# Performance work log

Hardware: AMD Instinct MI355X
Metric: run time of the kernel (lower is better)

## Reference

```python
import jax, jax.numpy as jnp
import numpy as np

EPS_LN = 1e-5  # torch nn.LayerNorm default

def layernorm(x, g, b):
    mu = x.mean(-1, keepdims=True)
    var = ((x - mu) ** 2).mean(-1, keepdims=True)
    return (x - mu) * jax.lax.rsqrt(var + EPS_LN) * g + b

def softmax_kernel(x, proj, is_query, kernel_eps=1e-4):
    # FAVOR+ positive softmax random features (performer_pytorch math).
    # x: (B,H,N,D) queries/keys, proj: (M,D) random projection.
    d = x.shape[-1]
    norm = d ** -0.25
    ratio = proj.shape[0] ** -0.5
    xd = jnp.einsum('bhnd,md->bhnm', x * norm, proj)
    diag = 0.5 * (x ** 2).sum(-1, keepdims=True) * (norm ** 2)  # (B,H,N,1)
    stab = jnp.max(xd, axis=-1, keepdims=True) if is_query else jnp.max(xd)
    return ratio * (jnp.exp(xd - diag - stab) + kernel_eps)

def linear_attention(q, k, v):
    # Non-causal O(N) attention. q,k: (B,H,N,M); v: (B,H,N,DH)
    k_sum = k.sum(axis=-2)                                      # (B,H,M)
    d_inv = 1.0 / jnp.einsum('bhnm,bhm->bhn', q, k_sum)
    context = jnp.einsum('bhnm,bhnd->bhmd', k, v)               # (B,H,M,DH)
    return jnp.einsum('bhnm,bhmd,bhn->bhnd', q, context, d_inv)

def setup_inputs():
    key = jax.random.key(0)
    B, K, D, H, L = 32, 2048, 256, 4, 2
    DH = D // H
    M = int(DH * np.log(DH))  # 266, performer_pytorch default nb_features
    FF = 4 * D
    ks = jax.random.split(key, 20)
    def w(i, shape):
        return jax.random.normal(ks[i], shape, dtype=jnp.float32) * 0.02
    return dict(
        expr=jax.random.uniform(ks[0], (B, K), dtype=jnp.float32),
        coords=jax.random.uniform(ks[1], (B, 2), dtype=jnp.float32),
        gene_emb=w(2, (K, D)), pos_emb=w(3, (K, D)),
        val_w=w(4, (1, D)), val_b=jnp.zeros((D,), jnp.float32),
        val_ln_g=jnp.ones((D,), jnp.float32), val_ln_b=jnp.zeros((D,), jnp.float32),
        sp_w=w(5, (2, D)), sp_b=jnp.zeros((D,), jnp.float32),
        sp_ln_g=jnp.ones((D,), jnp.float32), sp_ln_b=jnp.zeros((D,), jnp.float32),
        p_ln1_g=jnp.ones((L, D), jnp.float32), p_ln1_b=jnp.zeros((L, D), jnp.float32),
        p_wq=w(6, (L, D, D)), p_bq=jnp.zeros((L, D), jnp.float32),
        p_wk=w(7, (L, D, D)), p_bk=jnp.zeros((L, D), jnp.float32),
        p_wv=w(8, (L, D, D)), p_bv=jnp.zeros((L, D), jnp.float32),
        p_wo=w(9, (L, D, D)), p_bo=jnp.zeros((L, D), jnp.float32),
        p_ln2_g=jnp.ones((L, D), jnp.float32), p_ln2_b=jnp.zeros((L, D), jnp.float32),
        p_ff1_w=w(10, (L, D, FF)), p_ff1_b=jnp.zeros((L, FF), jnp.float32),
        p_ff2_w=w(11, (L, FF, D)), p_ff2_b=jnp.zeros((L, D), jnp.float32),
        proj=jax.random.normal(ks[12], (L, M, DH), dtype=jnp.float32),
        q_w=w(13, (D, D)), q_b=jnp.zeros((D,), jnp.float32),
        k_w=w(14, (D, D)), k_b=jnp.zeros((D,), jnp.float32),
        v_w=w(15, (D, D)), v_b=jnp.zeros((D,), jnp.float32),
        o_w=w(16, (D, D)), o_b=jnp.zeros((D,), jnp.float32),
    )

def reference(expr, coords, gene_emb, pos_emb, val_w, val_b, val_ln_g, val_ln_b,
              sp_w, sp_b, sp_ln_g, sp_ln_b,
              p_ln1_g, p_ln1_b, p_wq, p_bq, p_wk, p_bk, p_wv, p_bv, p_wo, p_bo,
              p_ln2_g, p_ln2_b, p_ff1_w, p_ff1_b, p_ff2_w, p_ff2_b, proj,
              q_w, q_b, k_w, k_b, v_w, v_b, o_w, o_b):
    B, K = expr.shape
    D = gene_emb.shape[1]
    L = p_wq.shape[0]
    H = 4
    DH = D // H
    # gene tokens = gene_id_emb + gene_pos_emb + GELU(LN(Linear(expr)))
    val = jax.nn.gelu(layernorm(expr[..., None] * val_w[0] + val_b, val_ln_g, val_ln_b), approximate=False)
    gene_tokens = (gene_emb + pos_emb)[None] + val                      # (B,K,D)
    sp = jax.nn.gelu(layernorm(coords @ sp_w + sp_b, sp_ln_g, sp_ln_b), approximate=False)
    x = jnp.concatenate([sp[:, None, :], gene_tokens], axis=1)          # (B,K+1,D)
    N = K + 1
    def split_heads(t):
        return t.reshape(B, N, H, DH).transpose(0, 2, 1, 3)
    # Performer: depth x [x + Attn(LN(x)); x + FF(LN(x))], dropout off (eval)
    for l in range(L):
        y = layernorm(x, p_ln1_g[l], p_ln1_b[l])
        q = split_heads(y @ p_wq[l] + p_bq[l])
        k = split_heads(y @ p_wk[l] + p_bk[l])
        v = split_heads(y @ p_wv[l] + p_bv[l])
        qf = softmax_kernel(q, proj[l], True)
        kf = softmax_kernel(k, proj[l], False)
        o = linear_attention(qf, kf, v)                                 # (B,H,N,DH)
        o = o.transpose(0, 2, 1, 3).reshape(B, N, D)
        x = x + (o @ p_wo[l] + p_bo[l])
        y = layernorm(x, p_ln2_g[l], p_ln2_b[l])
        x = x + (jax.nn.gelu(y @ p_ff1_w[l] + p_ff1_b[l], approximate=False) @ p_ff2_w[l] + p_ff2_b[l])
    # single-query cross-attention pooling: spatial token attends to genes
    spatial_out = x[:, :1]
    gene_out = x[:, 1:]
    q = spatial_out @ q_w + q_b                                          # (B,1,D)
    kk = gene_out @ k_w + k_b                                            # (B,K,D)
    vv = gene_out @ v_w + v_b
    attn = jax.nn.softmax(jnp.einsum('bqd,bkd->bqk', q, kk) / (D ** 0.5), axis=-1)
    pooled = jnp.einsum('bqk,bkd->bqd', attn, vv)[:, 0]                  # (B,D)
    return pooled @ o_w + o_b
```

## Files before the change

### kernel.cpp

```cpp
#include <hip/hip_runtime.h>
#include <hip/hip_bf16.h>
#include <math.h>

#define NB   32
#define KG   2048
#define NSEQ 2049
#define DIM  256
#define NH   4
#define DH   64
#define MF   266
#define FFD  1024
#define BN   (NB*NSEQ)
#define FFROWS2 32784
#define NORMC 0.35355339059327376f
#define RATIOC (1.0f/16.309506430300091f)

typedef __attribute__((ext_vector_type(8))) short short8;
typedef __attribute__((ext_vector_type(4))) float f32x4;
#define MFMA16(a,b,c) __builtin_amdgcn_mfma_f32_16x16x32_bf16(a,b,c,0,0,0)

__device__ __forceinline__ short f2b(float f){
  union{ __hip_bfloat16 h; short s;} u; u.h = __float2bfloat16(f); return u.s;
}
__device__ __forceinline__ float b2f(short s){
  union{ short s; __hip_bfloat16 h;} u; u.s = s; return __bfloat162float(u.h);
}
__device__ __forceinline__ float gelu_f(float x){
  return 0.5f*x*(1.0f+erff(x*0.70710678118654752f));
}
__device__ __forceinline__ void gload16(const short* g, short* l){
  __builtin_amdgcn_global_load_lds(
      (const __attribute__((address_space(1))) void*)g,
      (__attribute__((address_space(3))) void*)l, 16, 0, 0);
}
__device__ __forceinline__ float waveSum(float v){
  #pragma unroll
  for(int o=32;o>0;o>>=1) v += __shfl_down(v,o);
  return v;
}
__device__ __forceinline__ float waveMax(float v){
  #pragma unroll
  for(int o=32;o>0;o>>=1) v = fmaxf(v,__shfl_down(v,o));
  return v;
}
__device__ __forceinline__ float xorSum64(float v){
  v += __shfl_xor(v,32); v += __shfl_xor(v,16); v += __shfl_xor(v,8);
  v += __shfl_xor(v,4);  v += __shfl_xor(v,2);  v += __shfl_xor(v,1);
  return v;
}
__device__ __forceinline__ float blockSum256(float v, float* red){
  int lane = threadIdx.x & 63, wid = threadIdx.x >> 6;
  v = waveSum(v);
  __syncthreads();
  if(lane==0) red[wid]=v;
  __syncthreads();
  return red[0]+red[1]+red[2]+red[3];
}
__device__ __forceinline__ float blockMax256(float v, float* red){
  int lane = threadIdx.x & 63, wid = threadIdx.x >> 6;
  v = waveMax(v);
  __syncthreads();
  if(lane==0) red[wid]=v;
  __syncthreads();
  return fmaxf(fmaxf(red[0],red[1]),fmaxf(red[2],red[3]));
}
__device__ __forceinline__ unsigned fenc(float f){
  unsigned u = __float_as_uint(f);
  return (u & 0x80000000u) ? ~u : (u | 0x80000000u);
}
__device__ __forceinline__ float fdec(unsigned u){
  return (u & 0x80000000u) ? __uint_as_float(u & 0x7FFFFFFFu) : __uint_as_float(~u);
}

__global__ __launch_bounds__(256) void embed_kernel(
    const float* __restrict__ expr, const float* __restrict__ coords,
    const float* __restrict__ gene_emb, const float* __restrict__ pos_emb,
    const float* __restrict__ val_w, const float* __restrict__ val_b,
    const float* __restrict__ val_g, const float* __restrict__ val_bb,
    const float* __restrict__ sp_w, const float* __restrict__ sp_b,
    const float* __restrict__ sp_g, const float* __restrict__ sp_bb,
    const float* __restrict__ ln_g, const float* __restrict__ ln_b,
    float* __restrict__ x, short* __restrict__ ybf){
  int w = threadIdx.x >> 6, l = threadIdx.x & 63;
  int row = blockIdx.x*4 + w;
  int b = row / NSEQ, n = row % NSEQ;
  int d0 = l*4;
  float4 v;
  if(n==0){
    float c0 = coords[b*2], c1 = coords[b*2+1];
    float4 w0 = *reinterpret_cast<const float4*>(sp_w + d0);
    float4 w1 = *reinterpret_cast<const float4*>(sp_w + DIM + d0);
    float4 bb = *reinterpret_cast<const float4*>(sp_b + d0);
    v = make_float4(c0*w0.x+c1*w1.x+bb.x, c0*w0.y+c1*w1.y+bb.y,
                    c0*w0.z+c1*w1.z+bb.z, c0*w0.w+c1*w1.w+bb.w);
  } else {
    float e = expr[(size_t)b*KG + (n-1)];
    float4 vw = *reinterpret_cast<const float4*>(val_w + d0);
    float4 vb = *reinterpret_cast<const float4*>(val_b + d0);
    v = make_float4(e*vw.x+vb.x, e*vw.y+vb.y, e*vw.z+vb.z, e*vw.w+vb.w);
  }
  float mu = xorSum64(v.x+v.y+v.z+v.w)*(1.0f/DIM);
  float cx=v.x-mu, cy=v.y-mu, cz=v.z-mu, cw=v.w-mu;
  float var = xorSum64(cx*cx+cy*cy+cz*cz+cw*cw)*(1.0f/DIM);
  float r = rsqrtf(var + 1e-5f);
  float4 g  = (n==0)? *reinterpret_cast<const float4*>(sp_g + d0)
                    : *reinterpret_cast<const float4*>(val_g + d0);
  float4 be = (n==0)? *reinterpret_cast<const float4*>(sp_bb + d0)
                    : *reinterpret_cast<const float4*>(val_bb + d0);
  float4 h = make_float4(gelu_f(cx*r*g.x+be.x), gelu_f(cy*r*g.y+be.y),
                         gelu_f(cz*r*g.z+be.z), gelu_f(cw*r*g.w+be.w));
  if(n!=0){
    float4 ge = *reinterpret_cast<const float4*>(gene_emb + (size_t)(n-1)*DIM + d0);
    float4 pe = *reinterpret_cast<const float4*>(pos_emb  + (size_t)(n-1)*DIM + d0);
    h.x += ge.x+pe.x; h.y += ge.y+pe.y; h.z += ge.z+pe.z; h.w += ge.w+pe.w;
  }
  *reinterpret_cast<float4*>(x + (size_t)row*DIM + d0) = h;
  float s2 = xorSum64(h.x+h.y+h.z+h.w);
  float mu2 = s2*(1.0f/DIM);
  float c2x=h.x-mu2, c2y=h.y-mu2, c2z=h.z-mu2, c2w=h.w-mu2;
  float var2 = xorSum64(c2x*c2x+c2y*c2y+c2z*c2z+c2w*c2w)*(1.0f/DIM);
  float r2 = rsqrtf(var2+1e-5f);
  const float4 gv = *reinterpret_cast<const float4*>(ln_g + d0);
  const float4 bv = *reinterpret_cast<const float4*>(ln_b + d0);
  short4 o = make_short4(f2b(c2x*r2*gv.x+bv.x), f2b(c2y*r2*gv.y+bv.y),
                         f2b(c2z*r2*gv.z+bv.z), f2b(c2w*r2*gv.w+bv.w));
  *reinterpret_cast<short4*>(ybf + (size_t)row*DIM + d0) = o;
}

__global__ __launch_bounds__(256) void ln_bf4(const float* __restrict__ xin,
    const float* __restrict__ g, const float* __restrict__ bb, short* __restrict__ ybf){
  int w = threadIdx.x >> 6, l = threadIdx.x & 63;
  int row = blockIdx.x*4 + w;
  const float* xr = xin + (size_t)row*DIM;
  float4 v = *reinterpret_cast<const float4*>(xr + l*4);
  float s = xorSum64(v.x+v.y+v.z+v.w);
  float mu = s*(1.0f/DIM);
  float cx=v.x-mu, cy=v.y-mu, cz=v.z-mu, cw=v.w-mu;
  float var = xorSum64(cx*cx+cy*cy+cz*cz+cw*cw)*(1.0f/DIM);
  float r = rsqrtf(var+1e-5f);
  const float4 gv = *reinterpret_cast<const float4*>(g + l*4);
  const float4 bv = *reinterpret_cast<const float4*>(bb + l*4);
  short4 o = make_short4(f2b(cx*r*gv.x+bv.x), f2b(cy*r*gv.y+bv.y),
                         f2b(cz*r*gv.z+bv.z), f2b(cw*r*gv.w+bv.w));
  *reinterpret_cast<short4*>(ybf + (size_t)row*DIM + l*4) = o;
}

#define NW 14
struct WPArgs {
  const float* src[NW];
  short* dst[NW];
  int K[NW], N[NW];
  int ts[NW+1];
};
__global__ __launch_bounds__(256) void wprep_fused(WPArgs a){
  __shared__ float tile[32][33];
  int bx = blockIdx.x, t = threadIdx.x;
  int i = 0;
  while(bx >= a.ts[i+1]) i++;
  int tl = bx - a.ts[i];
  int N = a.N[i], K = a.K[i];
  int tcols = N >> 5;
  int tr = tl / tcols, tc = tl - tr*tcols;
  const float* src = a.src[i];
  short* dst = a.dst[i];
  int r = t>>3, c4 = (t&7)*4;
  float4 v = *reinterpret_cast<const float4*>(src + (size_t)(tr*32+r)*N + tc*32 + c4);
  tile[r][c4+0]=v.x; tile[r][c4+1]=v.y; tile[r][c4+2]=v.z; tile[r][c4+3]=v.w;
  __syncthreads();
  short4 o = make_short4(f2b(tile[c4+0][r]), f2b(tile[c4+1][r]),
                         f2b(tile[c4+2][r]), f2b(tile[c4+3][r]));
  *reinterpret_cast<short4*>(dst + (size_t)(tc*32+r)*K + tr*32 + c4) = o;
}

template<int EPI, int OBF, int WBF>
__global__ __launch_bounds__(256) void mgemm2(
    const short* __restrict__ A, const short* __restrict__ Bt,
    const float* __restrict__ bias, void* __restrict__ Cv,
    int M, int N, int Kd, short* __restrict__ Yb){
  __shared__ short As[128*64];
  __shared__ short Bs[128*64];
  int t=threadIdx.x, l=t&63, w=t>>6, lr=l&15, lk=l>>4;
  int wm=w>>1, wn=w&1;
  int m0=blockIdx.y*128, n0=blockIdx.x*128;
  f32x4 acc[4][4];
  #pragma unroll
  for(int i=0;i<4;i++)
    #pragma unroll
    for(int j=0;j<4;j++) acc[i][j]=f32x4{0.f,0.f,0.f,0.f};
  int rsw = (l>>3)&7;
  for(int k0=0;k0<Kd;k0+=64){
    #pragma unroll
    for(int p=0;p<4;p++){
      int chunk = p*256 + t;
      int row = chunk>>3, qc = chunk&7;
      short* lbase = &As[(size_t)(p*256 + w*64)*8];
      gload16(A + (size_t)(m0+row)*Kd + k0 + (qc^rsw)*8, lbase);
    }
    #pragma unroll
    for(int p=0;p<4;p++){
      int chunk = p*256 + t;
      int row = chunk>>3, qc = chunk&7;
      short* lbase = &Bs[(size_t)(p*256 + w*64)*8];
      gload16(Bt + (size_t)(n0+row)*Kd + k0 + (qc^rsw)*8, lbase);
    }
    __syncthreads();
    #pragma unroll
    for(int ks=0;ks<2;ks++){
      short8 af[4], bfr[4];
      #pragma unroll
      for(int i=0;i<4;i++)
        af[i] = *reinterpret_cast<const short8*>(&As[(wm*64+i*16+lr)*64 + ((ks*32+lk*8)^((lr&7)<<3))]);
      #pragma unroll
      for(int j=0;j<4;j++)
        bfr[j] = *reinterpret_cast<const short8*>(&Bs[(wn*64+j*16+lr)*64 + ((ks*32+lk*8)^((lr&7)<<3))]);
      #pragma unroll
      for(int i=0;i<4;i++)
        #pragma unroll
        for(int j=0;j<4;j++) acc[i][j] = MFMA16(af[i], bfr[j], acc[i][j]);
    }
    __syncthreads();
  }
  #pragma unroll
  for(int i=0;i<4;i++){
    int gm0 = m0 + wm*64 + i*16 + lk*4;
    #pragma unroll
    for(int j=0;j<4;j++){
      int gc = n0 + wn*64 + j*16 + lr;
      float bs = bias[gc];
      #pragma unroll
      for(int r=0;r<4;r++){
        int gm = gm0 + r;
        if(gm<M){
          float vv = acc[i][j][r] + bs;
          if(EPI==2) vv = gelu_f(vv);
          size_t idx = (size_t)gm*N + gc;
          if(OBF){
            ((short*)Cv)[idx] = f2b(vv);
          } else {
            float* C = (float*)Cv;
            if(EPI==1) vv += C[idx];
            C[idx] = vv;
            if(WBF) Yb[idx] = f2b(vv);
          }
        }
      }
    }
  }
}

__global__ __launch_bounds__(256) void qkv_gemm(
    const short* __restrict__ A, const short* __restrict__ Bt,
    const float* __restrict__ bq, const float* __restrict__ bk, const float* __restrict__ bv,
    short* __restrict__ qd, short* __restrict__ kd, short* __restrict__ vd,
    float* __restrict__ diagk, int M){
  __shared__ short As[128*64];
  __shared__ short Bs[128*64];
  int t=threadIdx.x, l=t&63, w=t>>6, lr=l&15, lk=l>>4;
  int wm=w>>1, wn=w&1;
  int m0=blockIdx.y*128, n0=blockIdx.x*128;
  f32x4 acc[4][4];
  #pragma unroll
  for(int i=0;i<4;i++)
    #pragma unroll
    for(int j=0;j<4;j++) acc[i][j]=f32x4{0.f,0.f,0.f,0.f};
  int rsw = (l>>3)&7;
  for(int k0=0;k0<DIM;k0+=64){
    #pragma unroll
    for(int p=0;p<4;p++){
      int chunk = p*256 + t;
      int row = chunk>>3, qc = chunk&7;
      short* lbase = &As[(size_t)(p*256 + w*64)*8];
      gload16(A + (size_t)(m0+row)*DIM + k0 + (qc^rsw)*8, lbase);
    }
    #pragma unroll
    for(int p=0;p<4;p++){
      int chunk = p*256 + t;
      int row = chunk>>3, qc = chunk&7;
      short* lbase = &Bs[(size_t)(p*256 + w*64)*8];
      gload16(Bt + (size_t)(n0+row)*DIM + k0 + (qc^rsw)*8, lbase);
    }
    __syncthreads();
    #pragma unroll
    for(int ks=0;ks<2;ks++){
      short8 af[4], bfr[4];
      #pragma unroll
      for(int i=0;i<4;i++)
        af[i] = *reinterpret_cast<const short8*>(&As[(wm*64+i*16+lr)*64 + ((ks*32+lk*8)^((lr&7)<<3))]);
      #pragma unroll
      for(int j=0;j<4;j++)
        bfr[j] = *reinterpret_cast<const short8*>(&Bs[(wn*64+j*16+lr)*64 + ((ks*32+lk*8)^((lr&7)<<3))]);
      #pragma unroll
      for(int i=0;i<4;i++)
        #pragma unroll
        for(int j=0;j<4;j++) acc[i][j] = MFMA16(af[i], bfr[j], acc[i][j]);
    }
    __syncthreads();
  }
  bool isK = (blockIdx.x==2) || (blockIdx.x==3);
  int headq = ((n0 + wn*64) - 256) >> 6;
  #pragma unroll
  for(int i=0;i<4;i++){
    int gm0 = m0 + wm*64 + i*16 + lk*4;
    float sq[4] = {0.f,0.f,0.f,0.f};
    #pragma unroll
    for(int j=0;j<4;j++){
      int gc = n0 + wn*64 + j*16 + lr;
      int sel = gc >> 8, col = gc & 255;
      short* dst = (sel==0)? qd : ((sel==1)? kd : vd);
      const float* bp = (sel==0)? bq : ((sel==1)? bk : bv);
      float bs = bp[col];
      #pragma unroll
      for(int r=0;r<4;r++){
        int gm = gm0 + r;
        if(gm<M){
          short sv = f2b(acc[i][j][r] + bs);
          dst[(size_t)gm*DIM + col] = sv;
          if(isK){ float kv = b2f(sv); sq[r] += kv*kv; }
        }
      }
    }
    if(isK){
      #pragma unroll
      for(int r=0;r<4;r++){
        float s = sq[r];
        s += __shfl_xor(s,1); s += __shfl_xor(s,2);
        s += __shfl_xor(s,4); s += __shfl_xor(s,8);
        if(lr==0){
          int gm = gm0 + r;
          if(gm<M){
            int bb_ = gm / NSEQ, nn_ = gm - bb_*NSEQ;
            diagk[((size_t)(bb_*NH+headq))*NSEQ + nn_] = 0.0625f*s;
          }
        }
      }
    }
  }
}

__global__ __launch_bounds__(256) void projprep_kernel(const float* __restrict__ proj,
    short* __restrict__ projbf, unsigned* __restrict__ kmax){
  int i = blockIdx.x*256 + threadIdx.x;
  if(i==0) *kmax = 0u;
  if(i < 320*64){
    int m = i>>6, d = i&63;
    float v = (m<MF)? proj[(size_t)m*DH + d]*NORMC : 0.f;
    projbf[i] = f2b(v);
  }
}

__global__ __launch_bounds__(256) void kside_max(
    const short* __restrict__ kbf, const short* __restrict__ projbf,
    unsigned* __restrict__ kmax){
  __shared__ short kS[32*72];
  __shared__ float red[4];
  int t=threadIdx.x, l=t&63, w=t>>6, lr=l&15, lk=l>>4;
  int split = blockIdx.x, bh = blockIdx.y;
  int b=bh>>2, h=bh&3;
  int c0 = split*9, c1 = min(c0+9, 65);
  int nf = (w==3)?5:4;
  short8 apf[5][2];
  #pragma unroll
  for(int fi=0;fi<5;fi++){
    int fr = (fi<4)? (fi*4+w) : 16;
    #pragma unroll
    for(int ks=0;ks<2;ks++)
      apf[fi][ks] = *reinterpret_cast<const short8*>(projbf + (fr*16+lr)*64 + ks*32 + lk*8);
  }
  const short8 z8 = {0,0,0,0,0,0,0,0};
  float lmax = -3.0e38f;
  for(int ch=c0; ch<c1; ++ch){
    int n0 = ch*32;
    __syncthreads();
    {
      int r = t>>3, c8 = (t&7)*8;
      int gn = n0 + r;
      short8 v8 = z8;
      if(gn<NSEQ) v8 = *reinterpret_cast<const short8*>(kbf + ((size_t)(b*NSEQ+gn))*DIM + h*DH + c8);
      *reinterpret_cast<short8*>(&kS[r*72+c8]) = v8;
    }
    __syncthreads();
    for(int fi=0;fi<nf;fi++){
      int fr = (fi<4)? (fi*4+w) : 16;
      #pragma unroll
      for(int fn=0;fn<2;fn++){
        f32x4 xa = f32x4{0.f,0.f,0.f,0.f};
        #pragma unroll
        for(int ks=0;ks<2;ks++){
          short8 bk = *reinterpret_cast<const short8*>(&kS[(fn*16+lr)*72 + ks*32 + lk*8]);
          xa = MFMA16(apf[fi][ks], bk, xa);
        }
        #pragma unroll
        for(int r=0;r<4;r++){
          int m = fr*16 + lk*4 + r;
          int n = n0 + fn*16 + lr;
          if(m<MF && n<NSEQ) lmax = fmaxf(lmax, xa[r]);
        }
      }
    }
  }
  float bm = blockMax256(lmax, red);
  if(t==0) atomicMax(kmax, fenc(bm));
}

__global__ __launch_bounds__(256) void kside_ctx(
    const short* __restrict__ kbf, const short* __restrict__ vbf,
    const short* __restrict__ projbf, const float* __restrict__ diagk,
    const unsigned* __restrict__ kmax, float* __restrict__ ctxP){
  __shared__ short kS[32*72];
  __shared__ short vT[64*40];
  __shared__ short kfS[80*40];
  __shared__ float diagS[32];
  int t=threadIdx.x, l=t&63, w=t>>6, lr=l&15, lk=l>>4;
  int fb=blockIdx.x&3, qh=blockIdx.x>>2, bh=blockIdx.y; int b=bh>>2, h=bh&3;
  int F0 = fb*5;
  int ch0 = qh*33, ch1 = min(65, ch0+33);
  float stab = fdec(*kmax);
  short8 apf0[2], apf1[2];
  #pragma unroll
  for(int ks=0;ks<2;ks++){
    apf0[ks] = *reinterpret_cast<const short8*>(projbf + ((F0+w)*16+lr)*64 + ks*32 + lk*8);
    apf1[ks] = *reinterpret_cast<const short8*>(projbf + ((F0+4)*16+lr)*64 + ks*32 + lk*8);
  }
  f32x4 ctx[5];
  #pragma unroll
  for(int f=0;f<5;f++) ctx[f]=f32x4{0.f,0.f,0.f,0.f};
  f32x4 ksc0 = f32x4{0.f,0.f,0.f,0.f};
  f32x4 ksc1 = f32x4{0.f,0.f,0.f,0.f};
  const short ONE=(short)0x3F80;
  const short8 ones8 = {ONE,ONE,ONE,ONE,ONE,ONE,ONE,ONE};
  const short8 z8 = {0,0,0,0,0,0,0,0};
  for(int ch=ch0; ch<ch1; ++ch){
    int n0 = ch*32;
    __syncthreads();
    {
      int r = t>>3, c8 = (t&7)*8;
      int gn = n0 + r;
      short8 v8 = z8;
      if(gn<NSEQ) v8 = *reinterpret_cast<const short8*>(kbf + ((size_t)(b*NSEQ+gn))*DIM + h*DH + c8);
      *reinterpret_cast<short8*>(&kS[r*72+c8]) = v8;
    }
    #pragma unroll
    for(int p=0;p<4;p++){
      int n2 = 2*w + 8*p;
      int dd = t&63;
      int gn0=n0+n2, gn1=gn0+1;
      short v0 = (gn0<NSEQ)? vbf[((size_t)(b*NSEQ+gn0))*DIM + h*DH + dd] : (short)0;
      short v1 = (gn1<NSEQ)? vbf[((size_t)(b*NSEQ+gn1))*DIM + h*DH + dd] : (short)0;
      *reinterpret_cast<short2*>(&vT[dd*40 + n2]) = make_short2(v0,v1);
    }
    if(t<32) diagS[t] = (n0+t<NSEQ)? diagk[(size_t)bh*NSEQ + n0+t] : 0.f;
    __syncthreads();
    #pragma unroll
    for(int fn=0;fn<2;fn++){
      f32x4 xa = f32x4{0.f,0.f,0.f,0.f};
      #pragma unroll
      for(int ks=0;ks<2;ks++){
        short8 bk = *reinterpret_cast<const short8*>(&kS[(fn*16+lr)*72 + ks*32 + lk*8]);
        xa = MFMA16(apf0[ks], bk, xa);
      }
      float dgn = diagS[fn*16+lr];
      #pragma unroll
      for(int r=0;r<4;r++){
        int m = (F0+w)*16 + lk*4 + r;
        int n = n0 + fn*16 + lr;
        float kf = (m<MF && n<NSEQ)? RATIOC*(__expf(xa[r]-dgn-stab)+1e-4f) : 0.f;
        kfS[(w*16+lk*4+r)*40 + fn*16 + lr] = f2b(kf);
      }
    }
    if(w==0){
      #pragma unroll
      for(int fn=0;fn<2;fn++){
        f32x4 xa = f32x4{0.f,0.f,0.f,0.f};
        #pragma unroll
        for(int ks=0;ks<2;ks++){
          short8 bk = *reinterpret_cast<const short8*>(&kS[(fn*16+lr)*72 + ks*32 + lk*8]);
          xa = MFMA16(apf1[ks], bk, xa);
        }
        float dgn = diagS[fn*16+lr];
        #pragma unroll
        for(int r=0;r<4;r++){
          int m = (F0+4)*16 + lk*4 + r;
          int n = n0 + fn*16 + lr;
          float kf = (m<MF && n<NSEQ)? RATIOC*(__expf(xa[r]-dgn-stab)+1e-4f) : 0.f;
          kfS[(64+lk*4+r)*40 + fn*16 + lr] = f2b(kf);
        }
      }
    }
    __syncthreads();
    short8 bv = *reinterpret_cast<const short8*>(&vT[(w*16+lr)*40 + lk*8]);
    short8 a0 = *reinterpret_cast<const short8*>(&kfS[(w*16+lr)*40 + lk*8]);
    short8 a4 = *reinterpret_cast<const short8*>(&kfS[(64+lr)*40 + lk*8]);
    ksc0 = MFMA16(a0, ones8, ksc0);
    ksc1 = MFMA16(a4, ones8, ksc1);
    #pragma unroll
    for(int fl=0;fl<5;fl++){
      short8 a_ = *reinterpret_cast<const short8*>(&kfS[(fl*16+lr)*40 + lk*8]);
      ctx[fl] = MFMA16(a_, bv, ctx[fl]);
    }
  }
  float* P = ctxP + ((size_t)(qh*128 + bh))*65*320;
  #pragma unroll
  for(int fl=0;fl<5;fl++){
    #pragma unroll
    for(int r=0;r<4;r++){
      int m = (F0+fl)*16 + lk*4 + r;
      P[(size_t)(w*16+lr)*320 + m] = ctx[fl][r];
    }
  }
  if(lr==0){
    #pragma unroll
    for(int r=0;r<4;r++){
      int m = (F0+w)*16 + lk*4 + r;
      P[(size_t)64*320 + m] = ksc0[r];
    }
    if(w==0){
      #pragma unroll
      for(int r=0;r<4;r++){
        int m = (F0+4)*16 + lk*4 + r;
        P[(size_t)64*320 + m] = ksc1[r];
      }
    }
  }
}

__global__ __launch_bounds__(256) void ctx_reduce(const float* __restrict__ ctxP, short* __restrict__ ctxT){
  int row = blockIdx.x, bh = blockIdx.y, t = threadIdx.x;
  short* o = ctxT + ((size_t)bh*80 + row)*288;
  if(row < 65){
    const float* P0 = ctxP + ((size_t)bh*65 + row)*320;
    const float* P1 = ctxP + ((size_t)(128+bh)*65 + row)*320;
    for(int m=t; m<288; m+=256)
      o[m] = (m<272)? f2b(P0[m]+P1[m]) : (short)0;
  } else {
    for(int m=t; m<288; m+=256) o[m] = 0;
  }
}

__global__ __launch_bounds__(256) void qside_mfma(
    const short* __restrict__ qbf, const short* __restrict__ projbf,
    const short* __restrict__ ctxT, short* __restrict__ obf){
  __shared__ short qfS[64*296];
  __shared__ float diagS[64];
  short* qS = qfS;
  int t=threadIdx.x, l=t&63, w=t>>6, lr=l&15, lk=l>>4;
  int n0 = blockIdx.x*64, bh = blockIdx.y;
  int b = bh>>2, h = bh&3;
  const short8 z8 = {0,0,0,0,0,0,0,0};
  {
    int r = t>>2, c8 = (t&3)*16;
    int gn = n0 + r;
    float ssq = 0.f;
    #pragma unroll
    for(int i=0;i<2;i++){
      short8 v8 = z8;
      if(gn<NSEQ) v8 = *reinterpret_cast<const short8*>(qbf + ((size_t)(b*NSEQ+gn))*DIM + h*DH + c8 + i*8);
      #pragma unroll
      for(int u=0;u<8;u++){ float fv=b2f(v8[u]); ssq += fv*fv; }
      *reinterpret_cast<short8*>(&qS[r*72+c8+i*8]) = v8;
    }
    ssq += __shfl_xor(ssq,1); ssq += __shfl_xor(ssq,2);
    if((t&3)==0) diagS[r] = 0.0625f*ssq;
  }
  short8 aq[2];
  #pragma unroll
  for(int ks=0;ks<2;ks++) aq[ks] = *reinterpret_cast<const short8*>(&qS[(w*16+lr)*72 + ks*32 + lk*8]);
  float dg[4];
  #pragma unroll
  for(int r=0;r<4;r++) dg[r] = diagS[w*16 + lk*4 + r];
  __syncthreads();
  {
    int pr = w*16 + (l>>2), pc = 272 + (l&3)*4;
    #pragma unroll
    for(int i=0;i<4;i++) qfS[pr*296 + pc + i] = 0;
  }
  f32x4 acc[17];
  #pragma unroll
  for(int f=0;f<17;f++) acc[f]=f32x4{0.f,0.f,0.f,0.f};
  #pragma unroll
  for(int f=0;f<17;f++){
    #pragma unroll
    for(int ks=0;ks<2;ks++){
      short8 bp = *reinterpret_cast<const short8*>(projbf + (f*16+lr)*64 + ks*32 + lk*8);
      acc[f] = MFMA16(aq[ks], bp, acc[f]);
    }
  }
  float rmax[4];
  #pragma unroll
  for(int r=0;r<4;r++){
    float m = -3.0e38f;
    #pragma unroll
    for(int f=0;f<17;f++){
      float v = (f==16 && lr>=10)? -3.0e38f : acc[f][r];
      m = fmaxf(m,v);
    }
    m = fmaxf(m,__shfl_xor(m,1)); m = fmaxf(m,__shfl_xor(m,2));
    m = fmaxf(m,__shfl_xor(m,4)); m = fmaxf(m,__shfl_xor(m,8));
    rmax[r]=m;
  }
  #pragma unroll
  for(int f=0;f<17;f++)
    #pragma unroll
    for(int r=0;r<4;r++){
      float qv = RATIOC*(__expf(acc[f][r] - dg[r] - rmax[r]) + 1e-4f);
      qfS[(w*16+lk*4+r)*296 + f*16 + lr] = f2b(qv);
    }
  f32x4 pv[5];
  #pragma unroll
  for(int f=0;f<5;f++) pv[f]=f32x4{0.f,0.f,0.f,0.f};
  const short* cT = ctxT + (size_t)bh*80*288;
  for(int ks=0;ks<9;ks++){
    short8 a_ = *reinterpret_cast<const short8*>(&qfS[(w*16+lr)*296 + ks*32 + lk*8]);
    #pragma unroll
    for(int f=0;f<5;f++){
      short8 bb = *reinterpret_cast<const short8*>(cT + (f*16+lr)*288 + ks*32 + lk*8);
      pv[f] = MFMA16(a_, bb, pv[f]);
    }
  }
  #pragma unroll
  for(int r=0;r<4;r++){
    int gn = n0 + w*16 + lk*4 + r;
    if(gn>=NSEQ) continue;
    float den = __shfl(pv[4][r], (l & 48), 64);
    float inv = 1.0f/den;
    size_t obase = ((size_t)(b*NSEQ+gn))*DIM + h*DH;
    #pragma unroll
    for(int f=0;f<4;f++) obf[obase + f*16 + lr] = f2b(pv[f][r]*inv);
  }
}

__global__ __launch_bounds__(256) void rowproj_kernel(const float* __restrict__ src,
    const float* __restrict__ W, const float* __restrict__ bias,
    float* __restrict__ dst, int rowstride){
  __shared__ float rs[DIM];
  int b=blockIdx.x, t=threadIdx.x;
  rs[t]=src[(size_t)b*rowstride+t];
  __syncthreads();
  float s=bias[t];
  for(int j=0;j<DIM;j++) s += rs[j]*W[(size_t)j*DIM+t];
  dst[(size_t)b*DIM+t]=s;
}

__global__ __launch_bounds__(256) void pool_scores(const float* __restrict__ qfin,
    const short* __restrict__ kk, float* __restrict__ scb){
  __shared__ float qsh[DIM];
  int kc=blockIdx.x, b=blockIdx.y, t=threadIdx.x;
  qsh[t]=qfin[b*DIM+t];
  __syncthreads();
  int kidx = kc*256 + t;
  const short* kr = kk + ((size_t)(b*NSEQ+1+kidx))*DIM;
  float s=0;
  for(int j8=0;j8<32;j8++){
    short8 kv = *reinterpret_cast<const short8*>(kr + j8*8);
    #pragma unroll
    for(int u=0;u<8;u++) s += qsh[j8*8+u]*b2f(kv[u]);
  }
  scb[(size_t)b*KG + kidx] = s*0.0625f;
}

__global__ __launch_bounds__(256) void pool_pv(const float* __restrict__ scb,
    const short* __restrict__ vv, float* __restrict__ pooled){
  __shared__ float sc[KG];
  __shared__ float red[4];
  int b=blockIdx.x, t=threadIdx.x;
  float ls[8]; float lmax=-3.4e38f;
  #pragma unroll
  for(int i=0;i<8;i++){
    ls[i] = scb[(size_t)b*KG + t + i*256];
    lmax = fmaxf(lmax, ls[i]);
  }
  float gmax=blockMax256(lmax,red);
  float lsum=0;
  #pragma unroll
  for(int i=0;i<8;i++){ float e=__expf(ls[i]-gmax); sc[t+i*256]=e; lsum+=e; }
  float gsum=blockSum256(lsum,red);
  __syncthreads();
  float inv=1.0f/gsum;
  float p=0;
  for(int kidx=0;kidx<KG;kidx++) p += sc[kidx]*b2f(vv[((size_t)(b*NSEQ+1+kidx))*DIM + t]);
  pooled[b*DIM+t]=p*inv;
}

extern "C" void kernel_launch(void* const* d_in, const int* in_sizes, int n_in,
                              void* d_out, int out_size, void* d_ws, size_t ws_size,
                              hipStream_t stream){
  const float* expr   =(const float*)d_in[0];
  const float* coords =(const float*)d_in[1];
  const float* gene_emb=(const float*)d_in[2];
  const float* pos_emb=(const float*)d_in[3];
  const float* val_w  =(const float*)d_in[4];
  const float* val_b  =(const float*)d_in[5];
  const float* val_g  =(const float*)d_in[6];
  const float* val_bb =(const float*)d_in[7];
  const float* sp_w   =(const float*)d_in[8];
  const float* sp_b   =(const float*)d_in[9];
  const float* sp_g   =(const float*)d_in[10];
  const float* sp_bb  =(const float*)d_in[11];
  const float* p_ln1_g=(const float*)d_in[12];
  const float* p_ln1_b=(const float*)d_in[13];
  const float* p_wq   =(const float*)d_in[14];
  const float* p_bq   =(const float*)d_in[15];
  const float* p_wk   =(const float*)d_in[16];
  const float* p_bk   =(const float*)d_in[17];
  const float* p_wv   =(const float*)d_in[18];
  const float* p_bv   =(const float*)d_in[19];
  const float* p_wo   =(const float*)d_in[20];
  const float* p_bo   =(const float*)d_in[21];
  const float* p_ln2_g=(const float*)d_in[22];
  const float* p_ln2_b=(const float*)d_in[23];
  const float* p_ff1_w=(const float*)d_in[24];
  const float* p_ff1_b=(const float*)d_in[25];
  const float* p_ff2_w=(const float*)d_in[26];
  const float* p_ff2_b=(const float*)d_in[27];
  const float* proj   =(const float*)d_in[28];
  const float* q_w    =(const float*)d_in[29];
  const float* q_b    =(const float*)d_in[30];
  const float* k_w    =(const float*)d_in[31];
  const float* k_b    =(const float*)d_in[32];
  const float* v_w    =(const float*)d_in[33];
  const float* v_b    =(const float*)d_in[34];
  const float* o_w    =(const float*)d_in[35];
  const float* o_b    =(const float*)d_in[36];
  float* out = (float*)d_out;

  const size_t BND = (size_t)BN*DIM;
  size_t needB = BND*4 + BND*2*4
               + ((size_t)NB*NH*NSEQ + 4 + 2*(size_t)NB*DIM)*4
               + ((size_t)20480 + 2949120 + 1703936)*2;
  if(ws_size < needB){
    hipMemsetAsync(d_out, 0, (size_t)out_size*sizeof(float), stream);
    return;
  }
  float* ws = (float*)d_ws;
  float* x  = ws;
  short* ybf = (short*)(x + BND);
  short* qbf = ybf + BND;
  short* kbf = qbf + BND;
  short* vbf = kbf + BND;
  float* diagk = (float*)(vbf + BND);
  unsigned* kmax = (unsigned*)(diagk + (size_t)NB*NH*NSEQ);
  float* qfin   = (float*)(kmax+4);
  float* pooled = qfin + NB*DIM;
  short* projbf = (short*)(pooled + NB*DIM);
  short* ctxT   = projbf + 20480;
  short* wt     = ctxT + (size_t)128*80*288;
  const size_t LW = 786432;
  float* ctxP = (float*)ybf;
  float* scb  = diagk;

  {
    WPArgs a;
    short* wtkk = wt + 2*LW;
    short* wtvv = wtkk + 65536;
    const float* s10[10] = {p_wq, p_wk, p_wv, p_wo,
                            p_wq+(size_t)DIM*DIM, p_wk+(size_t)DIM*DIM,
                            p_wv+(size_t)DIM*DIM, p_wo+(size_t)DIM*DIM,
                            k_w, v_w};
    short* d10[10] = {wt, wt+65536, wt+131072, wt+196608,
                      wt+LW, wt+LW+65536, wt+LW+131072, wt+LW+196608,
                      wtkk, wtvv};
    int ti = 0;
    for(int i=0;i<10;i++){
      a.src[i]=s10[i]; a.dst[i]=d10[i]; a.K[i]=DIM; a.N[i]=DIM;
      a.ts[i]=ti; ti+=64;
    }
    const float* sff[4] = {p_ff1_w, p_ff2_w, p_ff1_w+(size_t)DIM*FFD, p_ff2_w+(size_t)FFD*DIM};
    short* dff[4] = {wt+262144, wt+524288, wt+LW+262144, wt+LW+524288};
    int Kff[4] = {DIM, FFD, DIM, FFD};
    int Nff[4] = {FFD, DIM, FFD, DIM};
    for(int i=0;i<4;i++){
      a.src[10+i]=sff[i]; a.dst[10+i]=dff[i]; a.K[10+i]=Kff[i]; a.N[10+i]=Nff[i];
      a.ts[10+i]=ti; ti+=256;
    }
    a.ts[14]=ti;
    wprep_fused<<<1664,256,0,stream>>>(a);
  }

  embed_kernel<<<BN/4,256,0,stream>>>(expr,coords,gene_emb,pos_emb,val_w,val_b,val_g,val_bb,
                                      sp_w,sp_b,sp_g,sp_bb, p_ln1_g, p_ln1_b, x, ybf);

  dim3 gdd(2, (BN+127)/128);
  dim3 gqkv(6, (BN+127)/128);
  dim3 gff1(8, (FFROWS2+127)/128);
  dim3 gff2(2, (FFROWS2+127)/128);
  dim3 gkm(8, NB*NH);
  dim3 gkc(8, NB*NH);
  dim3 gcr(80, NB*NH);
  dim3 gq((NSEQ+63)/64, NB*NH);
  dim3 gps(8, NB);
  short* wtkk = wt + 2*LW;
  short* wtvv = wtkk + 65536;

  for(int l=0;l<2;l++){
    short* wl = wt + (size_t)l*LW;
    if(l>0) ln_bf4<<<BN/4,256,0,stream>>>(x, p_ln1_g+l*DIM, p_ln1_b+l*DIM, ybf);
    qkv_gemm<<<gqkv,256,0,stream>>>(ybf, wl, p_bq+l*DIM, p_bk+l*DIM, p_bv+l*DIM,
                                    qbf, kbf, vbf, diagk, BN);
    projprep_kernel<<<80,256,0,stream>>>(proj + (size_t)l*MF*DH, projbf, kmax);
    kside_max<<<gkm,256,0,stream>>>(kbf, projbf, kmax);
    kside_ctx<<<gkc,256,0,stream>>>(kbf, vbf, projbf, diagk, kmax, ctxP);
    ctx_reduce<<<gcr,256,0,stream>>>(ctxP, ctxT);
    qside_mfma<<<gq,256,0,stream>>>(qbf, projbf, ctxT, kbf);
    mgemm2<1,0,0><<<gdd,256,0,stream>>>(kbf, wl+196608, p_bo+l*DIM, x, BN, DIM, DIM, nullptr);
    ln_bf4<<<BN/4,256,0,stream>>>(x, p_ln2_g+l*DIM, p_ln2_b+l*DIM, ybf);
    for(int c2=0;c2<2;c2++){
      size_t roff=(size_t)c2*FFROWS2;
      mgemm2<2,1,0><<<gff1,256,0,stream>>>(ybf+roff*DIM, wl+262144, p_ff1_b+l*FFD, qbf,
                                           FFROWS2, FFD, DIM, nullptr);
      if(l==1)
        mgemm2<1,0,1><<<gff2,256,0,stream>>>(qbf, wl+524288, p_ff2_b+l*DIM, x+roff*DIM,
                                             FFROWS2, DIM, FFD, ybf+roff*DIM);
      else
        mgemm2<1,0,0><<<gff2,256,0,stream>>>(qbf, wl+524288, p_ff2_b+l*DIM, x+roff*DIM,
                                             FFROWS2, DIM, FFD, nullptr);
    }
  }

  mgemm2<0,1,0><<<gdd,256,0,stream>>>(ybf, wtkk, k_b, kbf, BN, DIM, DIM, nullptr);
  mgemm2<0,1,0><<<gdd,256,0,stream>>>(ybf, wtvv, v_b, vbf, BN, DIM, DIM, nullptr);
  rowproj_kernel<<<NB,256,0,stream>>>(x, q_w, q_b, qfin, NSEQ*DIM);
  pool_scores<<<gps,256,0,stream>>>(qfin, kbf, scb);
  pool_pv<<<NB,256,0,stream>>>(scb, vbf, pooled);
  rowproj_kernel<<<NB,256,0,stream>>>(pooled, o_w, o_b, out, DIM);
}
```

Baseline: 1.567 ms.

## Enlarge kside_ctx chunk to 64 rows with swizzled LDS loads; split pooling

```diff
diff --git a/kernel.cpp b/kernel.cpp
--- a/kernel.cpp
+++ b/kernel.cpp
@@ -406,14 +406,14 @@
     const short* __restrict__ kbf, const short* __restrict__ vbf,
     const short* __restrict__ projbf, const float* __restrict__ diagk,
     const unsigned* __restrict__ kmax, float* __restrict__ ctxP){
-  __shared__ short kS[32*72];
-  __shared__ short vT[64*40];
-  __shared__ short kfS[80*40];
-  __shared__ float diagS[32];
+  __shared__ short kS[64*64];
+  __shared__ short vT[64*72];
+  __shared__ short kfS[80*72];
+  __shared__ float diagS[64];
   int t=threadIdx.x, l=t&63, w=t>>6, lr=l&15, lk=l>>4;
   int fb=blockIdx.x&3, qh=blockIdx.x>>2, bh=blockIdx.y; int b=bh>>2, h=bh&3;
   int F0 = fb*5;
-  int ch0 = qh*33, ch1 = min(65, ch0+33);
+  int ch0 = qh*17, ch1 = min(33, ch0+17);
   float stab = fdec(*kmax);
   short8 apf0[2], apf1[2];
   #pragma unroll
@@ -428,34 +428,34 @@
   f32x4 ksc1 = f32x4{0.f,0.f,0.f,0.f};
   const short ONE=(short)0x3F80;
   const short8 ones8 = {ONE,ONE,ONE,ONE,ONE,ONE,ONE,ONE};
-  const short8 z8 = {0,0,0,0,0,0,0,0};
+  int rsw = (l>>3)&7;
   for(int ch=ch0; ch<ch1; ++ch){
-    int n0 = ch*32;
+    int n0 = ch*64;
     __syncthreads();
-    {
-      int r = t>>3, c8 = (t&7)*8;
-      int gn = n0 + r;
-      short8 v8 = z8;
-      if(gn<NSEQ) v8 = *reinterpret_cast<const short8*>(kbf + ((size_t)(b*NSEQ+gn))*DIM + h*DH + c8);
-      *reinterpret_cast<short8*>(&kS[r*72+c8]) = v8;
-    }
-    #pragma unroll
-    for(int p=0;p<4;p++){
+    #pragma unroll
+    for(int p=0;p<2;p++){
+      int chunk = p*256 + t;
+      int row = chunk>>3, qc = chunk&7;
+      short* lbase = &kS[(size_t)(p*256 + w*64)*8];
+      gload16(kbf + (size_t)(b*NSEQ + n0 + row)*DIM + h*DH + (qc^rsw)*8, lbase);
+    }
+    #pragma unroll
+    for(int p=0;p<8;p++){
       int n2 = 2*w + 8*p;
-      int dd = t&63;
+      int dd = l;
       int gn0=n0+n2, gn1=gn0+1;
       short v0 = (gn0<NSEQ)? vbf[((size_t)(b*NSEQ+gn0))*DIM + h*DH + dd] : (short)0;
       short v1 = (gn1<NSEQ)? vbf[((size_t)(b*NSEQ+gn1))*DIM + h*DH + dd] : (short)0;
-      *reinterpret_cast<short2*>(&vT[dd*40 + n2]) = make_short2(v0,v1);
-    }
-    if(t<32) diagS[t] = (n0+t<NSEQ)? diagk[(size_t)bh*NSEQ + n0+t] : 0.f;
+      *reinterpret_cast<short2*>(&vT[dd*72 + n2]) = make_short2(v0,v1);
+    }
+    if(t<64) diagS[t] = (n0+t<NSEQ)? diagk[(size_t)bh*NSEQ + n0+t] : 0.f;
     __syncthreads();
     #pragma unroll
-    for(int fn=0;fn<2;fn++){
+    for(int fn=0;fn<4;fn++){
       f32x4 xa = f32x4{0.f,0.f,0.f,0.f};
       #pragma unroll
       for(int ks=0;ks<2;ks++){
-        short8 bk = *reinterpret_cast<const short8*>(&kS[(fn*16+lr)*72 + ks*32 + lk*8]);
+        short8 bk = *reinterpret_cast<const short8*>(&kS[(fn*16+lr)*64 + ((ks*32+lk*8)^((lr&7)<<3))]);
         xa = MFMA16(apf0[ks], bk, xa);
       }
       float dgn = diagS[fn*16+lr];
@@ -464,16 +464,16 @@
         int m = (F0+w)*16 + lk*4 + r;
         int n = n0 + fn*16 + lr;
         float kf = (m<MF && n<NSEQ)? RATIOC*(__expf(xa[r]-dgn-stab)+1e-4f) : 0.f;
-        kfS[(w*16+lk*4+r)*40 + fn*16 + lr] = f2b(kf);
+        kfS[(w*16+lk*4+r)*72 + fn*16 + lr] = f2b(kf);
       }
     }
     if(w==0){
       #pragma unroll
-      for(int fn=0;fn<2;fn++){
+      for(int fn=0;fn<4;fn++){
         f32x4 xa = f32x4{0.f,0.f,0.f,0.f};
         #pragma unroll
         for(int ks=0;ks<2;ks++){
-          short8 bk = *reinterpret_cast<const short8*>(&kS[(fn*16+lr)*72 + ks*32 + lk*8]);
+          short8 bk = *reinterpret_cast<const short8*>(&kS[(fn*16+lr)*64 + ((ks*32+lk*8)^((lr&7)<<3))]);
           xa = MFMA16(apf1[ks], bk, xa);
         }
         float dgn = diagS[fn*16+lr];
@@ -482,20 +482,23 @@
           int m = (F0+4)*16 + lk*4 + r;
           int n = n0 + fn*16 + lr;
           float kf = (m<MF && n<NSEQ)? RATIOC*(__expf(xa[r]-dgn-stab)+1e-4f) : 0.f;
-          kfS[(64+lk*4+r)*40 + fn*16 + lr] = f2b(kf);
+          kfS[(64+lk*4+r)*72 + fn*16 + lr] = f2b(kf);
         }
       }
     }
     __syncthreads();
-    short8 bv = *reinterpret_cast<const short8*>(&vT[(w*16+lr)*40 + lk*8]);
-    short8 a0 = *reinterpret_cast<const short8*>(&kfS[(w*16+lr)*40 + lk*8]);
-    short8 a4 = *reinterpret_cast<const short8*>(&kfS[(64+lr)*40 + lk*8]);
-    ksc0 = MFMA16(a0, ones8, ksc0);
-    ksc1 = MFMA16(a4, ones8, ksc1);
-    #pragma unroll
-    for(int fl=0;fl<5;fl++){
-      short8 a_ = *reinterpret_cast<const short8*>(&kfS[(fl*16+lr)*40 + lk*8]);
-      ctx[fl] = MFMA16(a_, bv, ctx[fl]);
+    #pragma unroll
+    for(int ks2=0;ks2<2;ks2++){
+      short8 bv = *reinterpret_cast<const short8*>(&vT[(w*16+lr)*72 + ks2*32 + lk*8]);
+      short8 a0 = *reinterpret_cast<const short8*>(&kfS[(w*16+lr)*72 + ks2*32 + lk*8]);
+      short8 a4 = *reinterpret_cast<const short8*>(&kfS[(64+lr)*72 + ks2*32 + lk*8]);
+      ksc0 = MFMA16(a0, ones8, ksc0);
+      ksc1 = MFMA16(a4, ones8, ksc1);
+      #pragma unroll
+      for(int fl=0;fl<5;fl++){
+        short8 a_ = *reinterpret_cast<const short8*>(&kfS[(fl*16+lr)*72 + ks2*32 + lk*8]);
+        ctx[fl] = MFMA16(a_, bv, ctx[fl]);
+      }
     }
   }
   float* P = ctxP + ((size_t)(qh*128 + bh))*65*320;
@@ -657,9 +660,8 @@
   scb[(size_t)b*KG + kidx] = s*0.0625f;
 }
 
-__global__ __launch_bounds__(256) void pool_pv(const float* __restrict__ scb,
-    const short* __restrict__ vv, float* __restrict__ pooled){
-  __shared__ float sc[KG];
+__global__ __launch_bounds__(256) void pool_sm(const float* __restrict__ scb,
+    float* __restrict__ gms){
   __shared__ float red[4];
   int b=blockIdx.x, t=threadIdx.x;
   float ls[8]; float lmax=-3.4e38f;
@@ -671,13 +673,35 @@
   float gmax=blockMax256(lmax,red);
   float lsum=0;
   #pragma unroll
-  for(int i=0;i<8;i++){ float e=__expf(ls[i]-gmax); sc[t+i*256]=e; lsum+=e; }
+  for(int i=0;i<8;i++) lsum += __expf(ls[i]-gmax);
   float gsum=blockSum256(lsum,red);
+  if(t==0){ gms[b*2]=gmax; gms[b*2+1]=gsum; }
+}
+
+__global__ __launch_bounds__(256) void pool_pv2(const float* __restrict__ scb,
+    const float* __restrict__ gms, const short* __restrict__ vv,
+    float* __restrict__ part){
+  __shared__ float es[256];
+  int kc=blockIdx.x, b=blockIdx.y, t=threadIdx.x;
+  float gmax = gms[b*2];
+  es[t] = __expf(scb[(size_t)b*KG + kc*256 + t] - gmax);
   __syncthreads();
-  float inv=1.0f/gsum;
   float p=0;
-  for(int kidx=0;kidx<KG;kidx++) p += sc[kidx]*b2f(vv[((size_t)(b*NSEQ+1+kidx))*DIM + t]);
-  pooled[b*DIM+t]=p*inv;
+  for(int i=0;i<256;i++){
+    int kidx = kc*256 + i;
+    p += es[i] * b2f(vv[((size_t)(b*NSEQ+1+kidx))*DIM + t]);
+  }
+  part[((size_t)(b*8)+kc)*DIM + t] = p;
+}
+
+__global__ __launch_bounds__(256) void pool_fin(const float* __restrict__ part,
+    const float* __restrict__ gms, float* __restrict__ pooled){
+  int b=blockIdx.x, t=threadIdx.x;
+  float inv = 1.0f/gms[b*2+1];
+  float s=0;
+  #pragma unroll
+  for(int kc=0;kc<8;kc++) s += part[((size_t)(b*8)+kc)*DIM + t];
+  pooled[b*DIM+t] = s*inv;
 }
 
 extern "C" void kernel_launch(void* const* d_in, const int* in_sizes, int n_in,
@@ -746,6 +770,8 @@
   const size_t LW = 786432;
   float* ctxP = (float*)ybf;
   float* scb  = diagk;
+  float* gms  = diagk + 65536;
+  float* ppart= gms + 64;
 
   {
     WPArgs a;
@@ -819,6 +845,8 @@
   mgemm2<0,1,0><<<gdd,256,0,stream>>>(ybf, wtvv, v_b, vbf, BN, DIM, DIM, nullptr);
   rowproj_kernel<<<NB,256,0,stream>>>(x, q_w, q_b, qfin, NSEQ*DIM);
   pool_scores<<<gps,256,0,stream>>>(qfin, kbf, scb);
-  pool_pv<<<NB,256,0,stream>>>(scb, vbf, pooled);
+  pool_sm<<<NB,256,0,stream>>>(scb, gms);
+  pool_pv2<<<gps,256,0,stream>>>(scb, gms, vbf, ppart);
+  pool_fin<<<NB,256,0,stream>>>(ppart, gms, pooled);
   rowproj_kernel<<<NB,256,0,stream>>>(pooled, o_w, o_b, out, DIM);
 }
```

Measured after the change: 1.461 ms. -6.8%, faster.
